# Kernel optimization log

Hardware: AMD Instinct MI355X
Metric: run time of the kernel (lower is better)

Reference implementation:

```python
import jax, jax.numpy as jnp
import numpy as np

N, M, C = 2048, 32, 1024  # persons, max_others, dim_inner


def setup_inputs() -> dict:
    key = jax.random.key(0)
    k1, k2, k3, k4, k5, k6 = jax.random.split(key, 6)
    return {
        "person_features": jax.random.normal(k1, (N, C, 1, 1), dtype=jnp.float32),
        "other_features": jax.random.normal(k2, (N, M, C, 1, 1), dtype=jnp.float32),
        "person_boxes": jax.random.uniform(k3, (N, 4), dtype=jnp.float32),
        "other_boxes": jax.random.uniform(k4, (N, M, 4), dtype=jnp.float32),
        "is_person": jnp.ones((N, M), dtype=bool),
        "W": jax.random.normal(k5, (C, 2 * C), dtype=jnp.float32) / np.sqrt(2 * C),
        "b": jax.random.normal(k6, (C,), dtype=jnp.float32) * 0.01,
    }


def reference(person_features, other_features, person_boxes, other_boxes, is_person, W, b):
    # person_features: [n, c, 1, 1]; other_features: [n, m, c, 1, 1]
    p = person_features[:, :, 0, 0]        # [n, c]
    o = other_features[:, :, :, 0, 0]      # [n, m, c]
    # Linear on concat([p, o]) == p @ Wp^T + o @ Wo^T + b with W = [Wp | Wo]
    Wp, Wo = W[:, :p.shape[1]], W[:, p.shape[1]:]
    pk = jnp.einsum('nc,dc->nd', p, Wp)            # shared across others
    ok = jnp.einsum('nmc,dc->nmd', o, Wo)
    x = pk[:, None, :] + ok + b                    # [n, m, d]
    x = jnp.max(x, axis=1)                         # max-pool over others
    return x[:, :, None, None]                     # [n, d, 1, 1]
```

## Files before the change

### kernel.cpp

```cpp
#include <hip/hip_runtime.h>
#include <hip/hip_bf16.h>


#define NN 2048
#define MM 32
#define CC 1024

typedef __attribute__((ext_vector_type(8))) __bf16 bf16x8;
typedef __attribute__((ext_vector_type(4))) float f32x4;
typedef __attribute__((ext_vector_type(8))) unsigned short u16x8;
typedef __attribute__((ext_vector_type(4))) unsigned short u16x4;

__device__ inline unsigned short f2bf(float f) {
  union { __hip_bfloat16 h; unsigned short u; } v;
  v.h = __float2bfloat16(f);
  return v.u;
}

__device__ inline void gload_lds16(const void* g, void* l) {
  __builtin_amdgcn_global_load_lds(
      (const __attribute__((address_space(1))) void*)g,
      (__attribute__((address_space(3))) void*)l, 16, 0, 0);
}

__global__ void conv_pw(const float* __restrict__ p, const float* __restrict__ W,
                        unsigned short* __restrict__ pd,
                        unsigned short* __restrict__ wp,
                        unsigned short* __restrict__ wo) {
  const int PG = (NN * CC) / 8;
  const int WG = (CC * 2 * CC) / 8;
  int i = blockIdx.x * blockDim.x + threadIdx.x;
  int stride = gridDim.x * blockDim.x;
  for (; i < PG + WG; i += stride) {
    if (i < PG) {
      const float4* s = reinterpret_cast<const float4*>(p) + (size_t)i * 2;
      float4 a = s[0], b = s[1];
      u16x8 r;
      r[0] = f2bf(a.x); r[1] = f2bf(a.y); r[2] = f2bf(a.z); r[3] = f2bf(a.w);
      r[4] = f2bf(b.x); r[5] = f2bf(b.y); r[6] = f2bf(b.z); r[7] = f2bf(b.w);
      *reinterpret_cast<u16x8*>(pd + (size_t)i * 8) = r;
    } else {
      int f = i - PG;
      int e = f * 8;
      int d = e >> 11;
      int cc = e & 2047;
      const float4* s = reinterpret_cast<const float4*>(W) + (size_t)f * 2;
      float4 a = s[0], b = s[1];
      u16x8 r;
      r[0] = f2bf(a.x); r[1] = f2bf(a.y); r[2] = f2bf(a.z); r[3] = f2bf(a.w);
      r[4] = f2bf(b.x); r[5] = f2bf(b.y); r[6] = f2bf(b.z); r[7] = f2bf(b.w);
      unsigned short* o = (cc < CC) ? (wp + (size_t)d * CC + cc)
                                    : (wo + (size_t)d * CC + (cc - CC));
      *reinterpret_cast<u16x8*>(o) = r;
    }
  }
}

__global__ void gemm_pk(const unsigned short* __restrict__ A,
                        const unsigned short* __restrict__ B,
                        const float* __restrict__ bvec,
                        float* __restrict__ out) {
  __shared__ unsigned short As[128 * 64];
  __shared__ unsigned short Bs[128 * 64];

  int nb = gridDim.x;
  int chunk = nb >> 3;
  int obid = blockIdx.x;
  int vb = (obid & 7) * chunk + (obid >> 3);
  int bcol = vb & 7;
  int brow = vb >> 3;

  int tid = threadIdx.x;
  int l = tid & 63;
  int wid = tid >> 6;
  int wr = wid >> 1, wc = wid & 1;
  int lr = l & 15;
  int lk = (l >> 4) << 3;

  const unsigned short* gA = A + (size_t)brow * 128 * CC;
  const unsigned short* gB = B + (size_t)bcol * 128 * CC;

  f32x4 acc[4][4] = {};

  for (int kt = 0; kt < 16; ++kt) {
    int k0 = kt * 64;
#pragma unroll
    for (int j = 0; j < 4; ++j) {
      int f = (j * 256 + tid) * 8;
      int r = f >> 6;
      int c = f & 63;
      gload_lds16(gA + (size_t)r * CC + k0 + c, &As[f]);
      gload_lds16(gB + (size_t)r * CC + k0 + c, &Bs[f]);
    }
    __syncthreads();
#pragma unroll
    for (int kk = 0; kk < 2; ++kk) {
      bf16x8 af[4], bfr[4];
#pragma unroll
      for (int mi = 0; mi < 4; ++mi)
        af[mi] = *reinterpret_cast<const bf16x8*>(
            &As[(wr * 64 + mi * 16 + lr) * 64 + kk * 32 + lk]);
#pragma unroll
      for (int ni = 0; ni < 4; ++ni)
        bfr[ni] = *reinterpret_cast<const bf16x8*>(
            &Bs[(wc * 64 + ni * 16 + lr) * 64 + kk * 32 + lk]);
#pragma unroll
      for (int mi = 0; mi < 4; ++mi)
#pragma unroll
        for (int ni = 0; ni < 4; ++ni)
          acc[mi][ni] = __builtin_amdgcn_mfma_f32_16x16x32_bf16(
              af[mi], bfr[ni], acc[mi][ni], 0, 0, 0);
    }
    __syncthreads();
  }

#pragma unroll
  for (int mi = 0; mi < 4; ++mi) {
    int row = brow * 128 + wr * 64 + mi * 16 + (l >> 4) * 4;
#pragma unroll
    for (int ni = 0; ni < 4; ++ni) {
      int col = bcol * 128 + wc * 64 + ni * 16 + lr;
      float bb = bvec[col];
#pragma unroll
      for (int r = 0; r < 4; ++r)
        out[(size_t)(row + r) * CC + col] = acc[mi][ni][r] + bb;
    }
  }
}


#define BARRIER                                      \
  do {                                               \
    asm volatile("" ::: "memory");                   \
    __builtin_amdgcn_s_barrier();                    \
    asm volatile("" ::: "memory");                   \
  } while (0)

#define LGKM0 asm volatile("s_waitcnt lgkmcnt(0)" ::: "memory")
#define VMCNT(n) asm volatile("s_waitcnt vmcnt(" #n ")" ::: "memory")

#define STAGE_B(k0)                                                           \
  do {                                                                        \
    _Pragma("unroll") for (int j = 0; j < 4; ++j)                             \
        gload_lds16(gB + (size_t)(j * 32 + brr) * CC + (k0) + bsc,            \
                    lds + 16384 + (j * 256 + tid) * 16);                      \
  } while (0)

#define ISSUE_A(k0)                                                           \
  do {                                                                        \
    _Pragma("unroll") for (int j = 0; j < 8; ++j)                             \
        aL[j] = *reinterpret_cast<const float4*>(                             \
            gAf + (size_t)(j * 16 + arow0) * CC + (k0) + ac4 * 4);            \
  } while (0)

#define CVT_WRITE_A                                                           \
  do {                                                                        \
    _Pragma("unroll") for (int j = 0; j < 8; ++j) {                           \
      u16x4 r;                                                                \
      r[0] = f2bf(aL[j].x); r[1] = f2bf(aL[j].y);                             \
      r[2] = f2bf(aL[j].z); r[3] = f2bf(aL[j].w);                             \
      *reinterpret_cast<u16x4*>(lds + (j * 16 + arow0) * 128 + aswz) = r;     \
    }                                                                         \
  } while (0)

#define MFMA16X                                                               \
  do {                                                                        \
    __builtin_amdgcn_s_setprio(1);                                            \
    _Pragma("unroll") for (int mi = 0; mi < 4; ++mi)                          \
        _Pragma("unroll") for (int ni = 0; ni < 4; ++ni)                      \
            acc[mi][ni] = __builtin_amdgcn_mfma_f32_16x16x32_bf16(            \
                af[mi], bfr[ni], acc[mi][ni], 0, 0, 0);                       \
    __builtin_amdgcn_s_setprio(0);                                            \
  } while (0)

__global__ __launch_bounds__(256, 3) void gemm_fused(
    const float* __restrict__ A,
    const unsigned short* __restrict__ B,
    const float* __restrict__ pkb,
    float* __restrict__ out) {
  __shared__ char lds[32768];

  int obid = blockIdx.x;
  int vb = (obid & 7) * 512 + (obid >> 3);
  int bcol = vb & 7;
  int brow = vb >> 3;

  int tid = threadIdx.x;
  int l = tid & 63;
  int wid = tid >> 6;
  int wr = wid >> 1;
  int wc = wid & 1;
  int lr = l & 15;
  int g = l >> 4;

  const float* gAf = A + (size_t)brow * 128 * CC;
  const unsigned short* gB = B + (size_t)bcol * 128 * CC;

  int brr = tid >> 3;
  int bsc = ((tid & 7) ^ ((tid >> 3) & 7)) * 8;

  int arow0 = tid >> 4;
  int ac4 = tid & 15;
  int aswz = (((ac4 >> 1) ^ (arow0 & 7)) * 16) + (ac4 & 1) * 8;

  int axor = lr & 7;
  int a_k0 = (wr * 64 + lr) * 128 + ((g ^ axor) * 16);
  int a_k1 = (wr * 64 + lr) * 128 + (((4 + g) ^ axor) * 16);
  int b_k0 = 16384 + (wc * 64 + lr) * 128 + ((g ^ axor) * 16);
  int b_k1 = 16384 + (wc * 64 + lr) * 128 + (((4 + g) ^ axor) * 16);

  f32x4 acc[4][4] = {};
  bf16x8 af[4], bfr[4];
  float4 aL[8];

  ISSUE_A(0);

#pragma unroll 1
  for (int t = 0; t < 16; ++t) {
    BARRIER;
    VMCNT(0);
    CVT_WRITE_A;
    STAGE_B(t * 64);
    if (t + 1 < 16) ISSUE_A((t + 1) * 64);
    LGKM0;
    if (t + 1 < 16) { VMCNT(8); } else { VMCNT(0); }
    BARRIER;
#pragma unroll
    for (int mi = 0; mi < 4; ++mi)
      af[mi] = *(const bf16x8*)(lds + a_k0 + mi * 2048);
#pragma unroll
    for (int ni = 0; ni < 4; ++ni)
      bfr[ni] = *(const bf16x8*)(lds + b_k0 + ni * 2048);
    LGKM0;
    MFMA16X;
#pragma unroll
    for (int mi = 0; mi < 4; ++mi)
      af[mi] = *(const bf16x8*)(lds + a_k1 + mi * 2048);
#pragma unroll
    for (int ni = 0; ni < 4; ++ni)
      bfr[ni] = *(const bf16x8*)(lds + b_k1 + ni * 2048);
    LGKM0;
    MFMA16X;
  }

#pragma unroll
  for (int a = 0; a < 2; ++a) {
    int n = brow * 4 + wr * 2 + a;
#pragma unroll
    for (int ni = 0; ni < 4; ++ni) {
      float v = -3.402823466e38f;
#pragma unroll
      for (int mi = 2 * a; mi < 2 * a + 2; ++mi)
#pragma unroll
        for (int r = 0; r < 4; ++r) v = fmaxf(v, acc[mi][ni][r]);
      v = fmaxf(v, __shfl_xor(v, 16));
      v = fmaxf(v, __shfl_xor(v, 32));
      if (l < 16) {
        int col = bcol * 128 + wc * 64 + ni * 16 + l;
        out[(size_t)n * CC + col] = v + pkb[(size_t)n * CC + col];
      }
    }
  }
}

extern "C" void kernel_launch(void* const* d_in, const int* in_sizes, int n_in,
                              void* d_out, int out_size, void* d_ws, size_t ws_size,
                              hipStream_t stream) {
  const float* p = (const float*)d_in[0];
  const float* o = (const float*)d_in[1];
  const float* W = (const float*)d_in[5];
  const float* b = (const float*)d_in[6];
  float* out = (float*)d_out;

  char* ws = (char*)d_ws;
  unsigned short* p_bf  = (unsigned short*)ws;
  unsigned short* wp_bf = (unsigned short*)(ws + 4194304);
  unsigned short* wo_bf = (unsigned short*)(ws + 6291456);
  float*          pkb   = (float*)(ws + 8388608);

  conv_pw<<<512, 256, 0, stream>>>(p, W, p_bf, wp_bf, wo_bf);
  gemm_pk<<<128, 256, 0, stream>>>(p_bf, wp_bf, b, pkb);
  gemm_fused<<<4096, 256, 0, stream>>>(o, wo_bf, pkb, out);
}
```

Baseline: 195.8 us.

## Double-buffer B tiles in LDS to prefetch next K-step

Adds a second LDS buffer for the B operand so the next tile's B is loaded via global_load_lds while the current tile computes, removing the mid-iteration wait on B loads. The main loop is unrolled by two to alternate buffers. LDS per block grows from 32KB to 48KB, which can pressure occupancy at three blocks per CU.

```diff
diff --git a/kernel.cpp b/kernel.cpp
--- a/kernel.cpp
+++ b/kernel.cpp
@@ -139,11 +139,11 @@
 #define LGKM0 asm volatile("s_waitcnt lgkmcnt(0)" ::: "memory")
 #define VMCNT(n) asm volatile("s_waitcnt vmcnt(" #n ")" ::: "memory")
 
-#define STAGE_B(k0)                                                           \
+#define STAGE_B(bs, k0)                                                       \
   do {                                                                        \
     _Pragma("unroll") for (int j = 0; j < 4; ++j)                             \
         gload_lds16(gB + (size_t)(j * 32 + brr) * CC + (k0) + bsc,            \
-                    lds + 16384 + (j * 256 + tid) * 16);                      \
+                    lds + 16384 + (bs) * 16384 + (j * 256 + tid) * 16);       \
   } while (0)
 
 #define ISSUE_A(k0)                                                           \
@@ -173,12 +173,39 @@
     __builtin_amdgcn_s_setprio(0);                                            \
   } while (0)
 
+#define TILE(t, bs, nbs)                                                      \
+  do {                                                                        \
+    BARRIER;                      \
+    VMCNT(0);                         \
+    CVT_WRITE_A;                    \
+    if ((t) + 1 < 16) {                                                       \
+      STAGE_B(nbs, ((t) + 1) * 64);                       \
+      ISSUE_A(((t) + 1) * 64);                            \
+    }                                                                         \
+    LGKM0;                                         \
+    BARRIER;                              \
+    _Pragma("unroll") for (int mi = 0; mi < 4; ++mi)                          \
+        af[mi] = *(const bf16x8*)(lds + a_k0 + mi * 2048);                    \
+    _Pragma("unroll") for (int ni = 0; ni < 4; ++ni)                          \
+        bfr[ni] = *(const bf16x8*)(lds + 16384 + (bs) * 16384 + b_k0 +        \
+                                   ni * 2048);                                \
+    LGKM0;                                                                    \
+    MFMA16X;                                                                  \
+    _Pragma("unroll") for (int mi = 0; mi < 4; ++mi)                          \
+        af[mi] = *(const bf16x8*)(lds + a_k1 + mi * 2048);                    \
+    _Pragma("unroll") for (int ni = 0; ni < 4; ++ni)                          \
+        bfr[ni] = *(const bf16x8*)(lds + 16384 + (bs) * 16384 + b_k1 +        \
+                                   ni * 2048);                                \
+    LGKM0;                                                                    \
+    MFMA16X;                                                                  \
+  } while (0)
+
 __global__ __launch_bounds__(256, 3) void gemm_fused(
     const float* __restrict__ A,
     const unsigned short* __restrict__ B,
     const float* __restrict__ pkb,
     float* __restrict__ out) {
-  __shared__ char lds[32768];
+  __shared__ char lds[49152];
 
   int obid = blockIdx.x;
   int vb = (obid & 7) * 512 + (obid >> 3);
@@ -206,41 +233,20 @@
   int axor = lr & 7;
   int a_k0 = (wr * 64 + lr) * 128 + ((g ^ axor) * 16);
   int a_k1 = (wr * 64 + lr) * 128 + (((4 + g) ^ axor) * 16);
-  int b_k0 = 16384 + (wc * 64 + lr) * 128 + ((g ^ axor) * 16);
-  int b_k1 = 16384 + (wc * 64 + lr) * 128 + (((4 + g) ^ axor) * 16);
+  int b_k0 = (wc * 64 + lr) * 128 + ((g ^ axor) * 16);
+  int b_k1 = (wc * 64 + lr) * 128 + (((4 + g) ^ axor) * 16);
 
   f32x4 acc[4][4] = {};
   bf16x8 af[4], bfr[4];
   float4 aL[8];
 
+  STAGE_B(0, 0);
   ISSUE_A(0);
 
 #pragma unroll 1
-  for (int t = 0; t < 16; ++t) {
-    BARRIER;
-    VMCNT(0);
-    CVT_WRITE_A;
-    STAGE_B(t * 64);
-    if (t + 1 < 16) ISSUE_A((t + 1) * 64);
-    LGKM0;
-    if (t + 1 < 16) { VMCNT(8); } else { VMCNT(0); }
-    BARRIER;
-#pragma unroll
-    for (int mi = 0; mi < 4; ++mi)
-      af[mi] = *(const bf16x8*)(lds + a_k0 + mi * 2048);
-#pragma unroll
-    for (int ni = 0; ni < 4; ++ni)
-      bfr[ni] = *(const bf16x8*)(lds + b_k0 + ni * 2048);
-    LGKM0;
-    MFMA16X;
-#pragma unroll
-    for (int mi = 0; mi < 4; ++mi)
-      af[mi] = *(const bf16x8*)(lds + a_k1 + mi * 2048);
-#pragma unroll
-    for (int ni = 0; ni < 4; ++ni)
-      bfr[ni] = *(const bf16x8*)(lds + b_k1 + ni * 2048);
-    LGKM0;
-    MFMA16X;
+  for (int tt = 0; tt < 16; tt += 2) {
+    TILE(tt, 0, 1);
+    TILE(tt + 1, 1, 0);
   }
 
 #pragma unroll
```

Measured after the change: 406.1 us. +107.3%, slower.

## Load B fragments directly from global into registers, bypassing LDS

Applied to the files above, without the earlier changes.

B tiles are no longer staged into LDS with global_load_lds. Each wave now loads its B MFMA fragments straight from global memory into registers, which halves LDS use to 16 KB and drops the explicit vmcnt waits. This is meant to cut LDS traffic and let more blocks fit per CU. The cost is that B is read redundantly by the two waves sharing the same column half, and global latency now sits on the MFMA critical path, since the compiler must insert waits before the B registers are used.

```diff
diff --git a/kernel.cpp b/kernel.cpp
--- a/kernel.cpp
+++ b/kernel.cpp
@@ -137,14 +137,6 @@
   } while (0)
 
 #define LGKM0 asm volatile("s_waitcnt lgkmcnt(0)" ::: "memory")
-#define VMCNT(n) asm volatile("s_waitcnt vmcnt(" #n ")" ::: "memory")
-
-#define STAGE_B(k0)                                                           \
-  do {                                                                        \
-    _Pragma("unroll") for (int j = 0; j < 4; ++j)                             \
-        gload_lds16(gB + (size_t)(j * 32 + brr) * CC + (k0) + bsc,            \
-                    lds + 16384 + (j * 256 + tid) * 16);                      \
-  } while (0)
 
 #define ISSUE_A(k0)                                                           \
   do {                                                                        \
@@ -163,13 +155,20 @@
     }                                                                         \
   } while (0)
 
-#define MFMA16X                                                               \
+#define BLOAD(BF, t, kk)                                                      \
+  do {                                                                        \
+    _Pragma("unroll") for (int ni = 0; ni < 4; ++ni)                          \
+        BF[ni] = *reinterpret_cast<const bf16x8*>(                            \
+            gBw + (size_t)ni * 16 * CC + (t) * 64 + (kk) * 32 + g * 8);       \
+  } while (0)
+
+#define MFMA16X(BF)                                                           \
   do {                                                                        \
     __builtin_amdgcn_s_setprio(1);                                            \
     _Pragma("unroll") for (int mi = 0; mi < 4; ++mi)                          \
         _Pragma("unroll") for (int ni = 0; ni < 4; ++ni)                      \
             acc[mi][ni] = __builtin_amdgcn_mfma_f32_16x16x32_bf16(            \
-                af[mi], bfr[ni], acc[mi][ni], 0, 0, 0);                       \
+                af[mi], BF[ni], acc[mi][ni], 0, 0, 0);                        \
     __builtin_amdgcn_s_setprio(0);                                            \
   } while (0)
 
@@ -178,7 +177,7 @@
     const unsigned short* __restrict__ B,
     const float* __restrict__ pkb,
     float* __restrict__ out) {
-  __shared__ char lds[32768];
+  __shared__ char lds[16384];
 
   int obid = blockIdx.x;
   int vb = (obid & 7) * 512 + (obid >> 3);
@@ -194,10 +193,7 @@
   int g = l >> 4;
 
   const float* gAf = A + (size_t)brow * 128 * CC;
-  const unsigned short* gB = B + (size_t)bcol * 128 * CC;
-
-  int brr = tid >> 3;
-  int bsc = ((tid & 7) ^ ((tid >> 3) & 7)) * 8;
+  const unsigned short* gBw = B + (size_t)(bcol * 128 + wc * 64 + lr) * CC;
 
   int arow0 = tid >> 4;
   int ac4 = tid & 15;
@@ -206,11 +202,10 @@
   int axor = lr & 7;
   int a_k0 = (wr * 64 + lr) * 128 + ((g ^ axor) * 16);
   int a_k1 = (wr * 64 + lr) * 128 + (((4 + g) ^ axor) * 16);
-  int b_k0 = 16384 + (wc * 64 + lr) * 128 + ((g ^ axor) * 16);
-  int b_k1 = 16384 + (wc * 64 + lr) * 128 + (((4 + g) ^ axor) * 16);
 
   f32x4 acc[4][4] = {};
-  bf16x8 af[4], bfr[4];
+  bf16x8 af[4];
+  bf16x8 bfrA[4], bfrB[4];
   float4 aL[8];
 
   ISSUE_A(0);
@@ -218,29 +213,22 @@
 #pragma unroll 1
   for (int t = 0; t < 16; ++t) {
     BARRIER;
-    VMCNT(0);
     CVT_WRITE_A;
-    STAGE_B(t * 64);
+    BLOAD(bfrA, t, 0);
+    BLOAD(bfrB, t, 1);
     if (t + 1 < 16) ISSUE_A((t + 1) * 64);
     LGKM0;
-    if (t + 1 < 16) { VMCNT(8); } else { VMCNT(0); }
     BARRIER;
 #pragma unroll
     for (int mi = 0; mi < 4; ++mi)
       af[mi] = *(const bf16x8*)(lds + a_k0 + mi * 2048);
-#pragma unroll
-    for (int ni = 0; ni < 4; ++ni)
-      bfr[ni] = *(const bf16x8*)(lds + b_k0 + ni * 2048);
     LGKM0;
-    MFMA16X;
+    MFMA16X(bfrA);
 #pragma unroll
     for (int mi = 0; mi < 4; ++mi)
       af[mi] = *(const bf16x8*)(lds + a_k1 + mi * 2048);
-#pragma unroll
-    for (int ni = 0; ni < 4; ++ni)
-      bfr[ni] = *(const bf16x8*)(lds + b_k1 + ni * 2048);
     LGKM0;
-    MFMA16X;
+    MFMA16X(bfrB);
   }
 
 #pragma unroll
```

New measurement: 342.7 us. 75.0% more time.
